# Kernel tuning notes

Measured on AMD Instinct MI355X. Metric: run time of the kernel, lower is better.

## Reference

```python
import jax, jax.numpy as jnp
import numpy as np

IN_F = 1024
OUT_F = 2048
BATCH = 1024
LAMBD = 0.2
TOL = 1e-4
MAX_ITERS = 100


def setup_inputs() -> dict:
    key = jax.random.key(0)
    kx, kw = jax.random.split(key)
    x = jax.random.normal(kx, (BATCH, IN_F), dtype=jnp.float32)
    # weight init exactly as in torch __init__: randn then column-wise (dim=0) L2 normalization
    w = jax.random.normal(kw, (OUT_F, IN_F), dtype=jnp.float32)
    w = w / jnp.linalg.norm(w, axis=0)  # norm over out_features, broadcast over columns
    A = w.T  # (in, out)
    M = A.T @ A + jnp.eye(OUT_F, dtype=jnp.float32)  # (out, out)
    M_inv = jnp.linalg.inv(M).T
    return {"x": x, "weight": w, "M_inv": M_inv}


def _softshrink(z, lambd):
    return jnp.sign(z) * jnp.maximum(jnp.abs(z) - lambd, 0.0)


def _basis_pursuit_admm(A_dot_b, M_inv, lambd=LAMBD, tol=TOL, max_iters=MAX_ITERS):
    # Mask-based equivalent of the torch dynamic-resizing loop: solved rows are
    # frozen instead of removed; v_solution captures v at the iteration a row converges.
    B, Mdim = A_dot_b.shape
    z = jnp.zeros((B, Mdim), dtype=A_dot_b.dtype)
    solved0 = jnp.zeros((B,), dtype=bool)
    init = (z, z, z, z, solved0)  # v, u, v_prev, v_solution, solved

    def step(carry, _):
        v, u, v_prev, v_sol, solved = carry
        b_eff = A_dot_b + v - u                      # (B, M)
        xk = b_eff @ M_inv                           # (B, M) @ (M, M)
        v_new = _softshrink(xk + u, lambd)
        u_new = u + xk - v_new
        # negligible_improvement on the updated v vs previous v
        dx = jnp.linalg.norm(v_new - v_prev, axis=1)
        xn = jnp.linalg.norm(v_new, axis=1)
        conv = (dx / xn) < tol
        newly = conv & (~solved)
        v_sol = jnp.where(newly[:, None], v_new, v_sol)
        frozen = solved[:, None]
        v = jnp.where(frozen, v, v_new)
        u = jnp.where(frozen, u, u_new)
        solved = solved | newly
        return (v, u, v, v_sol, solved), None

    (v, u, v_prev, v_sol, solved), _ = jax.lax.scan(step, init, None, length=max_iters)
    # Matches torch: rows still unsolved after max_iters keep their initial zero solution.
    return v_sol


def reference(x, weight, M_inv):
    input_shape = x.shape
    b = jax.lax.stop_gradient(x.reshape(x.shape[0], -1))  # x.detach() in torch
    A_dot_b = b @ weight.T                                 # b.matmul(A) with A = weight.T
    encoded = _basis_pursuit_admm(A_dot_b, M_inv)
    decoded = encoded @ weight
    return encoded, decoded.reshape(input_shape)
```

## Files before the change

kernel.cpp:

```cpp
#include <hip/hip_runtime.h>
#include <math.h>

#define BATCH 1024
#define IN_F  1024
#define OUT_F 2048
#define LAMBD 0.2f
#define TOL   1e-4f
#define MAX_ITERS 100

#define KSPLIT 4
#define KCHUNK (OUT_F / KSPLIT)
#define BSCALE 32.0f
#define BSCALE_INV 0.03125f

typedef _Float16 half8 __attribute__((ext_vector_type(8)));
typedef _Float16 half4 __attribute__((ext_vector_type(4)));
typedef float    floatx16 __attribute__((ext_vector_type(16)));
typedef unsigned char fp8_t;

#define GLOAD_LDS16(g, l) __builtin_amdgcn_global_load_lds(              \
    (const __attribute__((address_space(1))) void*)(g),                  \
    (__attribute__((address_space(3))) void*)(l), 16, 0, 0)

__device__ inline int pk4_fp8(float a, float b, float c, float d) {
    int w = __builtin_amdgcn_cvt_pk_fp8_f32(a, b, 0, false);
    w = __builtin_amdgcn_cvt_pk_fp8_f32(c, d, w, true);
    return w;
}
__device__ inline fp8_t enc_fp8(float a) {
    return (fp8_t)(__builtin_amdgcn_cvt_pk_fp8_f32(a, a, 0, false) & 0xff);
}
__device__ inline void cvt4_fp8(int w, float o[4]) {
    o[0] = __builtin_amdgcn_cvt_f32_fp8(w, 0);
    o[1] = __builtin_amdgcn_cvt_f32_fp8(w, 1);
    o[2] = __builtin_amdgcn_cvt_f32_fp8(w, 2);
    o[3] = __builtin_amdgcn_cvt_f32_fp8(w, 3);
}

__global__ void init_kernel(float4* __restrict__ v16, float4* __restrict__ u16,
                            float4* __restrict__ enc, int* __restrict__ solved) {
    const int i = blockIdx.x * blockDim.x + threadIdx.x;
    const float4 z = make_float4(0.f, 0.f, 0.f, 0.f);
    const int nh = BATCH * OUT_F / 8;
    const int n4 = BATCH * OUT_F / 4;
    if (i < nh) { v16[i] = z; u16[i] = z; }
    if (i < n4) enc[i] = z;
    if (i < BATCH) solved[i] = 0;
}

__global__ __launch_bounds__(256)
void cast_f16_kernel(const float* __restrict__ in, _Float16* __restrict__ out, int n) {
    const int i = (blockIdx.x * 256 + threadIdx.x) * 4;
    if (i < n) {
        const float4 f = *(const float4*)&in[i];
        half4 h;
        h[0] = (_Float16)f.x; h[1] = (_Float16)f.y;
        h[2] = (_Float16)f.z; h[3] = (_Float16)f.w;
        *(half4*)&out[i] = h;
    }
}

__global__ __launch_bounds__(256)
void transpose_w_kernel(const float* __restrict__ W, _Float16* __restrict__ WT) {
    __shared__ float tile[32][33];
    const int tid = threadIdx.x;
    const int row0 = blockIdx.y * 32;
    const int col0 = blockIdx.x * 32;
    const int r = tid >> 3;
    const int c4 = (tid & 7) * 4;
    const float4 b4 = *(const float4*)&W[(size_t)(row0 + r) * IN_F + col0 + c4];
    tile[r][c4 + 0] = b4.x; tile[r][c4 + 1] = b4.y;
    tile[r][c4 + 2] = b4.z; tile[r][c4 + 3] = b4.w;
    __syncthreads();
    half4 h;
#pragma unroll
    for (int j = 0; j < 4; ++j) h[j] = (_Float16)tile[c4 + j][r];
    *(half4*)&WT[(size_t)(col0 + r) * OUT_F + row0 + c4] = h;
}

__global__ __launch_bounds__(256)
void split_b_kernel(const float* __restrict__ B, fp8_t* __restrict__ BhT) {
    __shared__ float tile[32][33];
    const int tid = threadIdx.x;
    const int k0 = blockIdx.y * 32;
    const int n0 = blockIdx.x * 32;
    const int r = tid >> 3;
    const int c4 = (tid & 7) * 4;
    const float4 b4 = *(const float4*)&B[(size_t)(k0 + r) * OUT_F + n0 + c4];
    tile[r][c4 + 0] = b4.x; tile[r][c4 + 1] = b4.y;
    tile[r][c4 + 2] = b4.z; tile[r][c4 + 3] = b4.w;
    __syncthreads();
    const int w = pk4_fp8(tile[c4 + 0][r] * BSCALE, tile[c4 + 1][r] * BSCALE,
                          tile[c4 + 2][r] * BSCALE, tile[c4 + 3][r] * BSCALE);
    *(int*)&BhT[(size_t)(n0 + r) * OUT_F + k0 + c4] = w;
}

__global__ __launch_bounds__(256)
void mfma_nt_ab(const _Float16* __restrict__ A, const _Float16* __restrict__ B,
                fp8_t* __restrict__ Ab8, fp8_t* __restrict__ Ah,
                int N, int K) {
    __shared__ _Float16 sA[128 * 32];
    __shared__ _Float16 sB[128 * 32];
    const int tid = threadIdx.x;
    const int m0 = blockIdx.y * 128;
    const int n0 = blockIdx.x * 128;
    const int wv = tid >> 6, ln = tid & 63;
    const int half = ln >> 5, l31 = ln & 31;
    const int wm = (wv >> 1) * 64, wn = (wv & 1) * 64;
    const int r0 = tid >> 2, koff = (tid & 3) * 8;
    const size_t ga0 = (size_t)(m0 + r0) * K + koff;
    const size_t ga1 = (size_t)(m0 + r0 + 64) * K + koff;
    const size_t gb0 = (size_t)(n0 + r0) * K + koff;
    const size_t gb1 = (size_t)(n0 + r0 + 64) * K + koff;
    const int ldst0 = tid * 8, ldst1 = (256 + tid) * 8;

    floatx16 acc[2][2];
#pragma unroll
    for (int a = 0; a < 2; ++a)
#pragma unroll
        for (int b = 0; b < 2; ++b)
#pragma unroll
            for (int q = 0; q < 16; ++q) acc[a][b][q] = 0.f;

    for (int k = 0; k < K; k += 32) {
        __syncthreads();
        GLOAD_LDS16(A + ga0 + k, sA + ldst0);
        GLOAD_LDS16(A + ga1 + k, sA + ldst1);
        GLOAD_LDS16(B + gb0 + k, sB + ldst0);
        GLOAD_LDS16(B + gb1 + k, sB + ldst1);
        __syncthreads();
#pragma unroll
        for (int kk = 0; kk < 2; ++kk) {
            const int ko = kk * 16 + half * 8;
            const half8 a0 = *(const half8*)&sA[(wm + l31) * 32 + ko];
            const half8 a1 = *(const half8*)&sA[(wm + 32 + l31) * 32 + ko];
            const half8 b0 = *(const half8*)&sB[(wn + l31) * 32 + ko];
            const half8 b1 = *(const half8*)&sB[(wn + 32 + l31) * 32 + ko];
            acc[0][0] = __builtin_amdgcn_mfma_f32_32x32x16_f16(a0, b0, acc[0][0], 0, 0, 0);
            acc[0][1] = __builtin_amdgcn_mfma_f32_32x32x16_f16(a0, b1, acc[0][1], 0, 0, 0);
            acc[1][0] = __builtin_amdgcn_mfma_f32_32x32x16_f16(a1, b0, acc[1][0], 0, 0, 0);
            acc[1][1] = __builtin_amdgcn_mfma_f32_32x32x16_f16(a1, b1, acc[1][1], 0, 0, 0);
        }
    }
#pragma unroll
    for (int mm = 0; mm < 2; ++mm)
#pragma unroll
        for (int nn = 0; nn < 2; ++nn) {
            const int col = n0 + wn + nn * 32 + l31;
#pragma unroll
            for (int q = 0; q < 16; ++q) {
                const int row = m0 + wm + mm * 32 + (q & 3) + 8 * (q >> 2) + 4 * half;
                const size_t o = (size_t)row * N + col;
                const fp8_t e = enc_fp8(acc[mm][nn][q]);
                Ab8[o] = e;
                Ah[o] = e;
            }
        }
}

__global__ __launch_bounds__(256)
void mfma_nn_dec(const _Float16* __restrict__ A, const _Float16* __restrict__ B,
                 float* __restrict__ C, int N, int K) {
    __shared__ _Float16 sA[128 * 32];
    __shared__ _Float16 sB[128 * 32];
    const int tid = threadIdx.x;
    const int m0 = blockIdx.y * 128;
    const int n0 = blockIdx.x * 128;
    const int wv = tid >> 6, ln = tid & 63;
    const int half = ln >> 5, l31 = ln & 31;
    const int wm = (wv >> 1) * 64, wn = (wv & 1) * 64;
    const int r0 = tid >> 2, koff = (tid & 3) * 8;
    const size_t ga0 = (size_t)(m0 + r0) * K + koff;
    const size_t ga1 = (size_t)(m0 + r0 + 64) * K + koff;
    const size_t gb0 = (size_t)(n0 + r0) * K + koff;
    const size_t gb1 = (size_t)(n0 + r0 + 64) * K + koff;
    const int ldst0 = tid * 8, ldst1 = (256 + tid) * 8;

    floatx16 acc[2][2];
#pragma unroll
    for (int a = 0; a < 2; ++a)
#pragma unroll
        for (int b = 0; b < 2; ++b)
#pragma unroll
            for (int q = 0; q < 16; ++q) acc[a][b][q] = 0.f;

    for (int k = 0; k < K; k += 32) {
        __syncthreads();
        GLOAD_LDS16(A + ga0 + k, sA + ldst0);
        GLOAD_LDS16(A + ga1 + k, sA + ldst1);
        GLOAD_LDS16(B + gb0 + k, sB + ldst0);
        GLOAD_LDS16(B + gb1 + k, sB + ldst1);
        __syncthreads();
#pragma unroll
        for (int kk = 0; kk < 2; ++kk) {
            const int ko = kk * 16 + half * 8;
            const half8 a0 = *(const half8*)&sA[(wm + l31) * 32 + ko];
            const half8 a1 = *(const half8*)&sA[(wm + 32 + l31) * 32 + ko];
            const half8 b0 = *(const half8*)&sB[(wn + l31) * 32 + ko];
            const half8 b1 = *(const half8*)&sB[(wn + 32 + l31) * 32 + ko];
            acc[0][0] = __builtin_amdgcn_mfma_f32_32x32x16_f16(a0, b0, acc[0][0], 0, 0, 0);
            acc[0][1] = __builtin_amdgcn_mfma_f32_32x32x16_f16(a0, b1, acc[0][1], 0, 0, 0);
            acc[1][0] = __builtin_amdgcn_mfma_f32_32x32x16_f16(a1, b0, acc[1][0], 0, 0, 0);
            acc[1][1] = __builtin_amdgcn_mfma_f32_32x32x16_f16(a1, b1, acc[1][1], 0, 0, 0);
        }
    }
#pragma unroll
    for (int mm = 0; mm < 2; ++mm)
#pragma unroll
        for (int nn = 0; nn < 2; ++nn) {
            const int col = n0 + wn + nn * 32 + l31;
#pragma unroll
            for (int q = 0; q < 16; ++q) {
                const int row = m0 + wm + mm * 32 + (q & 3) + 8 * (q >> 2) + 4 * half;
                C[(size_t)row * N + col] = acc[mm][nn][q];
            }
        }
}

__global__ __launch_bounds__(256)
void xk_mfma(const fp8_t* __restrict__ Ah, const fp8_t* __restrict__ BhT,
             fp8_t* __restrict__ xkp, const int* __restrict__ solved) {
    __shared__ fp8_t smem[16384];
    fp8_t* sA = smem;
    fp8_t* sB = smem + 8192;
    const int tid = threadIdx.x;
    const int m0 = blockIdx.y * 128;
    const int n0 = blockIdx.x * 128;
    const int kz = blockIdx.z;
    constexpr size_t P = (size_t)BATCH * OUT_F;

    __shared__ int s_active;
    if (tid == 0) s_active = 0;
    __syncthreads();
    if (tid < 128 && solved[m0 + tid] == 0) s_active = 1;
    __syncthreads();
    if (!s_active) return;

    const int wv = tid >> 6;
    const int ln = tid & 63;
    const int half = ln >> 5;
    const int l31 = ln & 31;
    const int wm = (wv >> 1) * 64;
    const int wn = (wv & 1) * 64;

    const int r = tid & 127;
    const int c0 = tid >> 7;
    const fp8_t* gA = Ah  + (size_t)(m0 + r) * OUT_F + kz * KCHUNK;
    const fp8_t* gB = BhT + (size_t)(n0 + r) * OUT_F + kz * KCHUNK;
    fp8_t* lA0 = sA + (c0 * 128 + r) * 16;
    fp8_t* lA1 = sA + ((c0 + 2) * 128 + r) * 16;
    fp8_t* lB0 = sB + (c0 * 128 + r) * 16;
    fp8_t* lB1 = sB + ((c0 + 2) * 128 + r) * 16;

    floatx16 acc[2][2];
#pragma unroll
    for (int a = 0; a < 2; ++a)
#pragma unroll
        for (int b = 0; b < 2; ++b)
#pragma unroll
            for (int q = 0; q < 16; ++q) acc[a][b][q] = 0.f;

    const int ao0 = (wm + l31) * 16 + half * 8;
    const int ao1 = (wm + 32 + l31) * 16 + half * 8;
    const int bo0 = (wn + l31) * 16 + half * 8;
    const int bo1 = (wn + 32 + l31) * 16 + half * 8;

    for (int k = 0; k < KCHUNK; k += 64) {
        __syncthreads();
        GLOAD_LDS16(gA + k + c0 * 16, lA0);
        GLOAD_LDS16(gA + k + (c0 + 2) * 16, lA1);
        GLOAD_LDS16(gB + k + c0 * 16, lB0);
        GLOAD_LDS16(gB + k + (c0 + 2) * 16, lB1);
        __syncthreads();

#pragma unroll
        for (int kk = 0; kk < 4; ++kk) {
            const int cb = kk * 2048;
            const long long a0 = *(const long long*)&sA[cb + ao0];
            const long long a1 = *(const long long*)&sA[cb + ao1];
            const long long b0 = *(const long long*)&sB[cb + bo0];
            const long long b1 = *(const long long*)&sB[cb + bo1];
            acc[0][0] = __builtin_amdgcn_mfma_f32_32x32x16_fp8_fp8(a0, b0, acc[0][0], 0, 0, 0);
            acc[0][1] = __builtin_amdgcn_mfma_f32_32x32x16_fp8_fp8(a0, b1, acc[0][1], 0, 0, 0);
            acc[1][0] = __builtin_amdgcn_mfma_f32_32x32x16_fp8_fp8(a1, b0, acc[1][0], 0, 0, 0);
            acc[1][1] = __builtin_amdgcn_mfma_f32_32x32x16_fp8_fp8(a1, b1, acc[1][1], 0, 0, 0);
        }
    }

    __syncthreads();
#pragma unroll
    for (int mm = 0; mm < 2; ++mm)
#pragma unroll
        for (int nn = 0; nn < 2; ++nn) {
            const int lcol = wn + nn * 32 + l31;
#pragma unroll
            for (int q = 0; q < 16; ++q) {
                const int lrow = wm + mm * 32 + (q & 3) + 8 * (q >> 2) + 4 * half;
                smem[lrow * 128 + lcol] = enc_fp8(acc[mm][nn][q] * BSCALE_INV);
            }
        }
    __syncthreads();
    fp8_t* outp = xkp + kz * P + (size_t)m0 * OUT_F + n0;
#pragma unroll
    for (int s = 0; s < 4; ++s) {
        const int f = (s * 256 + tid) * 16;
        *(int4*)&outp[(size_t)(f >> 7) * OUT_F + (f & 127)] = *(const int4*)&smem[f];
    }
}

__global__ __launch_bounds__(256)
void update_kernel(const fp8_t* __restrict__ xkp, const fp8_t* __restrict__ Ab8,
                   _Float16* __restrict__ v, _Float16* __restrict__ u,
                   float* __restrict__ enc, fp8_t* __restrict__ Ah,
                   int* __restrict__ solved) {
    const int row = blockIdx.x;
    if (solved[row]) return;
    const int t = threadIdx.x;
    constexpr size_t P = (size_t)BATCH * OUT_F;

    const int c = t * 8;
    const size_t off = (size_t)row * OUT_F + c;
    const int2 q0 = *(const int2*)&xkp[off];
    const int2 q1 = *(const int2*)&xkp[P + off];
    const int2 q2 = *(const int2*)&xkp[2 * P + off];
    const int2 q3 = *(const int2*)&xkp[3 * P + off];
    const half8 u8 = *(const half8*)&u[off];
    const half8 v8 = *(const half8*)&v[off];
    const int2 ab2 = *(const int2*)&Ab8[off];

    float f0[4], f1[4], f2[4], f3[4], g0[4], g1[4], g2[4], g3[4];
    cvt4_fp8(q0.x, f0); cvt4_fp8(q1.x, f1); cvt4_fp8(q2.x, f2); cvt4_fp8(q3.x, f3);
    cvt4_fp8(q0.y, g0); cvt4_fp8(q1.y, g1); cvt4_fp8(q2.y, g2); cvt4_fp8(q3.y, g3);
    float ab0[4], ab1[4];
    cvt4_fp8(ab2.x, ab0); cvt4_fp8(ab2.y, ab1);
    float xs[8], abv[8];
#pragma unroll
    for (int j = 0; j < 4; ++j) {
        xs[j] = f0[j] + f1[j] + f2[j] + f3[j];
        xs[j + 4] = g0[j] + g1[j] + g2[j] + g3[j];
        abv[j] = ab0[j];
        abv[j + 4] = ab1[j];
    }

    float vn_all[8], ae[8];
    half8 vo, uo;
    float dx2 = 0.f, xn2 = 0.f;
#pragma unroll
    for (int j = 0; j < 8; ++j) {
        const float xk = xs[j];
        const float uv = (float)u8[j];
        const float vp = (float)v8[j];
        const float z = xk + uv;
        const float az = fabsf(z) - LAMBD;
        const float vnew = az > 0.f ? copysignf(az, z) : 0.f;
        const float unew = uv + xk - vnew;
        const float d = vnew - vp;
        dx2 += d * d;
        xn2 += vnew * vnew;
        vn_all[j] = vnew;
        vo[j] = (_Float16)vnew;
        uo[j] = (_Float16)unew;
        ae[j] = abv[j] + vnew - unew;
    }
    *(half8*)&v[off] = vo;
    *(half8*)&u[off] = uo;
    int2 ah;
    ah.x = pk4_fp8(ae[0], ae[1], ae[2], ae[3]);
    ah.y = pk4_fp8(ae[4], ae[5], ae[6], ae[7]);
    *(int2*)&Ah[off] = ah;

#pragma unroll
    for (int o = 32; o > 0; o >>= 1) {
        dx2 += __shfl_down(dx2, o);
        xn2 += __shfl_down(xn2, o);
    }
    __shared__ float sdx[4], sxn[4];
    __shared__ float s_conv;
    if ((t & 63) == 0) { sdx[t >> 6] = dx2; sxn[t >> 6] = xn2; }
    __syncthreads();
    if (t == 0) {
        const float dxt = sqrtf(sdx[0] + sdx[1] + sdx[2] + sdx[3]);
        const float xnt = sqrtf(sxn[0] + sxn[1] + sxn[2] + sxn[3]);
        const bool conv = (dxt / xnt) < TOL;
        s_conv = conv ? 1.f : 0.f;
        if (conv) solved[row] = 1;
    }
    __syncthreads();
    if (s_conv != 0.f) {
        *(float4*)&enc[off] = make_float4(vn_all[0], vn_all[1], vn_all[2], vn_all[3]);
        *(float4*)&enc[off + 4] = make_float4(vn_all[4], vn_all[5], vn_all[6], vn_all[7]);
    }
}

extern "C" void kernel_launch(void* const* d_in, const int* in_sizes, int n_in,
                              void* d_out, int out_size, void* d_ws, size_t ws_size,
                              hipStream_t stream) {
    (void)in_sizes; (void)n_in; (void)out_size; (void)ws_size;
    const float* x    = (const float*)d_in[0];
    const float* w    = (const float*)d_in[1];
    const float* Minv = (const float*)d_in[2];

    float* enc = (float*)d_out;
    float* dec = enc + (size_t)BATCH * OUT_F;

    constexpr size_t P = (size_t)BATCH * OUT_F;
    fp8_t* Ab8 = (fp8_t*)d_ws;
    _Float16* v   = (_Float16*)(Ab8 + P);
    _Float16* u   = v + P;
    _Float16* xh  = u + P;
    _Float16* wh  = xh + (size_t)BATCH * IN_F;
    _Float16* whT = wh + (size_t)OUT_F * IN_F;
    _Float16* ench = whT + (size_t)IN_F * OUT_F;
    fp8_t* Ah  = (fp8_t*)(ench + P);
    fp8_t* xkp = Ah + P;
    fp8_t* BhT = xkp + 4 * P;
    int* solved = (int*)(BhT + (size_t)OUT_F * OUT_F);

    {
        const int n = BATCH * OUT_F / 4;
        init_kernel<<<(n + 255) / 256, 256, 0, stream>>>(
            (float4*)v, (float4*)u, (float4*)enc, solved);
    }

    split_b_kernel<<<dim3(OUT_F / 32, OUT_F / 32), 256, 0, stream>>>(Minv, BhT);

    cast_f16_kernel<<<(BATCH * IN_F / 4 + 255) / 256, 256, 0, stream>>>(x, xh, BATCH * IN_F);
    cast_f16_kernel<<<(OUT_F * IN_F / 4 + 255) / 256, 256, 0, stream>>>(w, wh, OUT_F * IN_F);
    transpose_w_kernel<<<dim3(IN_F / 32, OUT_F / 32), 256, 0, stream>>>(w, whT);

    mfma_nt_ab<<<dim3(OUT_F / 128, BATCH / 128), 256, 0, stream>>>(
        xh, wh, Ab8, Ah, OUT_F, IN_F);

    for (int it = 0; it < MAX_ITERS; ++it) {
        xk_mfma<<<dim3(OUT_F / 128, BATCH / 128, KSPLIT), 256, 0, stream>>>(
            Ah, BhT, xkp, solved);
        update_kernel<<<BATCH, 256, 0, stream>>>(xkp, Ab8, v, u, enc, Ah, solved);
    }

    cast_f16_kernel<<<(BATCH * OUT_F / 4 + 255) / 256, 256, 0, stream>>>(enc, ench, BATCH * OUT_F);
    mfma_nn_dec<<<dim3(IN_F / 128, BATCH / 128), 256, 0, stream>>>(
        ench, whT, dec, IN_F, OUT_F);
}
```

Measured before the change: 2.261 ms.

## Compact unsolved rows into a list so the GEMM runs only on active tiles

The update kernel now builds a compacted, double-buffered list of unsolved batch rows and a count. Block 0 does this with a prefix-sum scan and pads the list to a multiple of 128. The xk GEMM gathers A rows through this list and launches only enough row-tiles to cover the active count. Before, a 128-row tile was skipped only if every row in it was solved. The cost is an indirect row gather, a serial compaction in one block, and a list that can lag by one iteration because block 0 reads `solved` while other blocks are still updating it. The per-row `solved` check in the update kernel keeps that lag from corrupting results.

```diff
diff --git a/kernel.cpp b/kernel.cpp
--- a/kernel.cpp
+++ b/kernel.cpp
@@ -38,14 +38,16 @@
 }
 
 __global__ void init_kernel(float4* __restrict__ v16, float4* __restrict__ u16,
-                            float4* __restrict__ enc, int* __restrict__ solved) {
+                            float4* __restrict__ enc, int* __restrict__ solved,
+                            int* __restrict__ list0, int* __restrict__ cnts) {
     const int i = blockIdx.x * blockDim.x + threadIdx.x;
     const float4 z = make_float4(0.f, 0.f, 0.f, 0.f);
     const int nh = BATCH * OUT_F / 8;
     const int n4 = BATCH * OUT_F / 4;
     if (i < nh) { v16[i] = z; u16[i] = z; }
     if (i < n4) enc[i] = z;
-    if (i < BATCH) solved[i] = 0;
+    if (i < BATCH) { solved[i] = 0; list0[i] = i; }
+    if (i < 2) cnts[i] = BATCH;
 }
 
 __global__ __launch_bounds__(256)
@@ -219,22 +221,19 @@
 
 __global__ __launch_bounds__(256)
 void xk_mfma(const fp8_t* __restrict__ Ah, const fp8_t* __restrict__ BhT,
-             fp8_t* __restrict__ xkp, const int* __restrict__ solved) {
+             fp8_t* __restrict__ xkp, const int* __restrict__ list_cur,
+             const int* __restrict__ cnt_cur) {
+    const int cnt = *cnt_cur;
+    const int m0 = blockIdx.y * 128;
+    if (m0 >= cnt) return;
+
     __shared__ fp8_t smem[16384];
     fp8_t* sA = smem;
     fp8_t* sB = smem + 8192;
     const int tid = threadIdx.x;
-    const int m0 = blockIdx.y * 128;
     const int n0 = blockIdx.x * 128;
     const int kz = blockIdx.z;
     constexpr size_t P = (size_t)BATCH * OUT_F;
-
-    __shared__ int s_active;
-    if (tid == 0) s_active = 0;
-    __syncthreads();
-    if (tid < 128 && solved[m0 + tid] == 0) s_active = 1;
-    __syncthreads();
-    if (!s_active) return;
 
     const int wv = tid >> 6;
     const int ln = tid & 63;
@@ -245,7 +244,8 @@
 
     const int r = tid & 127;
     const int c0 = tid >> 7;
-    const fp8_t* gA = Ah  + (size_t)(m0 + r) * OUT_F + kz * KCHUNK;
+    const int arow = list_cur[m0 + r];
+    const fp8_t* gA = Ah  + (size_t)arow * OUT_F + kz * KCHUNK;
     const fp8_t* gB = BhT + (size_t)(n0 + r) * OUT_F + kz * KCHUNK;
     fp8_t* lA0 = sA + (c0 * 128 + r) * 16;
     fp8_t* lA1 = sA + ((c0 + 2) * 128 + r) * 16;
@@ -312,83 +312,136 @@
 void update_kernel(const fp8_t* __restrict__ xkp, const fp8_t* __restrict__ Ab8,
                    _Float16* __restrict__ v, _Float16* __restrict__ u,
                    float* __restrict__ enc, fp8_t* __restrict__ Ah,
-                   int* __restrict__ solved) {
-    const int row = blockIdx.x;
-    if (solved[row]) return;
+                   int* __restrict__ solved,
+                   const int* __restrict__ list_cur, int* __restrict__ list_nxt,
+                   const int* __restrict__ cnt_cur, int* __restrict__ cnt_nxt) {
+    const int cnt = *cnt_cur;
+    const int p = blockIdx.x;
     const int t = threadIdx.x;
+    if (p >= cnt && p != 0) return;
     constexpr size_t P = (size_t)BATCH * OUT_F;
 
-    const int c = t * 8;
-    const size_t off = (size_t)row * OUT_F + c;
-    const int2 q0 = *(const int2*)&xkp[off];
-    const int2 q1 = *(const int2*)&xkp[P + off];
-    const int2 q2 = *(const int2*)&xkp[2 * P + off];
-    const int2 q3 = *(const int2*)&xkp[3 * P + off];
-    const half8 u8 = *(const half8*)&u[off];
-    const half8 v8 = *(const half8*)&v[off];
-    const int2 ab2 = *(const int2*)&Ab8[off];
-
-    float f0[4], f1[4], f2[4], f3[4], g0[4], g1[4], g2[4], g3[4];
-    cvt4_fp8(q0.x, f0); cvt4_fp8(q1.x, f1); cvt4_fp8(q2.x, f2); cvt4_fp8(q3.x, f3);
-    cvt4_fp8(q0.y, g0); cvt4_fp8(q1.y, g1); cvt4_fp8(q2.y, g2); cvt4_fp8(q3.y, g3);
-    float ab0[4], ab1[4];
-    cvt4_fp8(ab2.x, ab0); cvt4_fp8(ab2.y, ab1);
-    float xs[8], abv[8];
-#pragma unroll
-    for (int j = 0; j < 4; ++j) {
-        xs[j] = f0[j] + f1[j] + f2[j] + f3[j];
-        xs[j + 4] = g0[j] + g1[j] + g2[j] + g3[j];
-        abv[j] = ab0[j];
-        abv[j + 4] = ab1[j];
-    }
-
-    float vn_all[8], ae[8];
-    half8 vo, uo;
-    float dx2 = 0.f, xn2 = 0.f;
-#pragma unroll
-    for (int j = 0; j < 8; ++j) {
-        const float xk = xs[j];
-        const float uv = (float)u8[j];
-        const float vp = (float)v8[j];
-        const float z = xk + uv;
-        const float az = fabsf(z) - LAMBD;
-        const float vnew = az > 0.f ? copysignf(az, z) : 0.f;
-        const float unew = uv + xk - vnew;
-        const float d = vnew - vp;
-        dx2 += d * d;
-        xn2 += vnew * vnew;
-        vn_all[j] = vnew;
-        vo[j] = (_Float16)vnew;
-        uo[j] = (_Float16)unew;
-        ae[j] = abv[j] + vnew - unew;
-    }
-    *(half8*)&v[off] = vo;
-    *(half8*)&u[off] = uo;
-    int2 ah;
-    ah.x = pk4_fp8(ae[0], ae[1], ae[2], ae[3]);
-    ah.y = pk4_fp8(ae[4], ae[5], ae[6], ae[7]);
-    *(int2*)&Ah[off] = ah;
-
-#pragma unroll
-    for (int o = 32; o > 0; o >>= 1) {
-        dx2 += __shfl_down(dx2, o);
-        xn2 += __shfl_down(xn2, o);
-    }
     __shared__ float sdx[4], sxn[4];
     __shared__ float s_conv;
-    if ((t & 63) == 0) { sdx[t >> 6] = dx2; sxn[t >> 6] = xn2; }
-    __syncthreads();
-    if (t == 0) {
-        const float dxt = sqrtf(sdx[0] + sdx[1] + sdx[2] + sdx[3]);
-        const float xnt = sqrtf(sxn[0] + sxn[1] + sxn[2] + sxn[3]);
-        const bool conv = (dxt / xnt) < TOL;
-        s_conv = conv ? 1.f : 0.f;
-        if (conv) solved[row] = 1;
-    }
-    __syncthreads();
-    if (s_conv != 0.f) {
-        *(float4*)&enc[off] = make_float4(vn_all[0], vn_all[1], vn_all[2], vn_all[3]);
-        *(float4*)&enc[off + 4] = make_float4(vn_all[4], vn_all[5], vn_all[6], vn_all[7]);
+    __shared__ int wbase[5];
+
+    const bool dowork = (p < cnt);
+    int row = 0;
+    bool active = false;
+    if (dowork) {
+        row = list_cur[p];
+        active = (solved[row] == 0);
+    }
+
+    if (active) {
+        const int c = t * 8;
+        const size_t offp = (size_t)p * OUT_F + c;
+        const size_t off  = (size_t)row * OUT_F + c;
+        const int2 q0 = *(const int2*)&xkp[offp];
+        const int2 q1 = *(const int2*)&xkp[P + offp];
+        const int2 q2 = *(const int2*)&xkp[2 * P + offp];
+        const int2 q3 = *(const int2*)&xkp[3 * P + offp];
+        const half8 u8 = *(const half8*)&u[off];
+        const half8 v8 = *(const half8*)&v[off];
+        const int2 ab2 = *(const int2*)&Ab8[off];
+
+        float f0[4], f1[4], f2[4], f3[4], g0[4], g1[4], g2[4], g3[4];
+        cvt4_fp8(q0.x, f0); cvt4_fp8(q1.x, f1); cvt4_fp8(q2.x, f2); cvt4_fp8(q3.x, f3);
+        cvt4_fp8(q0.y, g0); cvt4_fp8(q1.y, g1); cvt4_fp8(q2.y, g2); cvt4_fp8(q3.y, g3);
+        float ab0[4], ab1[4];
+        cvt4_fp8(ab2.x, ab0); cvt4_fp8(ab2.y, ab1);
+        float xs[8], abv[8];
+#pragma unroll
+        for (int j = 0; j < 4; ++j) {
+            xs[j] = f0[j] + f1[j] + f2[j] + f3[j];
+            xs[j + 4] = g0[j] + g1[j] + g2[j] + g3[j];
+            abv[j] = ab0[j];
+            abv[j + 4] = ab1[j];
+        }
+
+        float vn_all[8], ae[8];
+        half8 vo, uo;
+        float dx2 = 0.f, xn2 = 0.f;
+#pragma unroll
+        for (int j = 0; j < 8; ++j) {
+            const float xk = xs[j];
+            const float uv = (float)u8[j];
+            const float vp = (float)v8[j];
+            const float z = xk + uv;
+            const float az = fabsf(z) - LAMBD;
+            const float vnew = az > 0.f ? copysignf(az, z) : 0.f;
+            const float unew = uv + xk - vnew;
+            const float d = vnew - vp;
+            dx2 += d * d;
+            xn2 += vnew * vnew;
+            vn_all[j] = vnew;
+            vo[j] = (_Float16)vnew;
+            uo[j] = (_Float16)unew;
+            ae[j] = abv[j] + vnew - unew;
+        }
+        *(half8*)&v[off] = vo;
+        *(half8*)&u[off] = uo;
+        int2 ah;
+        ah.x = pk4_fp8(ae[0], ae[1], ae[2], ae[3]);
+        ah.y = pk4_fp8(ae[4], ae[5], ae[6], ae[7]);
+        *(int2*)&Ah[off] = ah;
+
+#pragma unroll
+        for (int o = 32; o > 0; o >>= 1) {
+            dx2 += __shfl_down(dx2, o);
+            xn2 += __shfl_down(xn2, o);
+        }
+        if ((t & 63) == 0) { sdx[t >> 6] = dx2; sxn[t >> 6] = xn2; }
+        __syncthreads();
+        if (t == 0) {
+            const float dxt = sqrtf(sdx[0] + sdx[1] + sdx[2] + sdx[3]);
+            const float xnt = sqrtf(sxn[0] + sxn[1] + sxn[2] + sxn[3]);
+            const bool conv = (dxt / xnt) < TOL;
+            s_conv = conv ? 1.f : 0.f;
+            if (conv) solved[row] = 1;
+        }
+        __syncthreads();
+        if (s_conv != 0.f) {
+            *(float4*)&enc[off] = make_float4(vn_all[0], vn_all[1], vn_all[2], vn_all[3]);
+            *(float4*)&enc[off + 4] = make_float4(vn_all[4], vn_all[5], vn_all[6], vn_all[7]);
+        }
+    }
+
+    if (p == 0) {
+        const int lane = t & 63;
+        const int wv = t >> 6;
+        int m = 0;
+#pragma unroll
+        for (int j = 0; j < 4; ++j) {
+            const int rr = t * 4 + j;
+            if (solved[rr] == 0) m |= 1 << j;
+        }
+        const int c4 = __popc(m);
+        int inc = c4;
+#pragma unroll
+        for (int off = 1; off < 64; off <<= 1) {
+            const int x = __shfl_up(inc, off);
+            if (lane >= off) inc += x;
+        }
+        const int exc = inc - c4;
+        if (lane == 63) wbase[wv] = inc;
+        __syncthreads();
+        if (t == 0) {
+            int s = 0;
+#pragma unroll
+            for (int w = 0; w < 4; ++w) { const int x = wbase[w]; wbase[w] = s; s += x; }
+            wbase[4] = s;
+        }
+        __syncthreads();
+        int pos = wbase[wv] + exc;
+#pragma unroll
+        for (int j = 0; j < 4; ++j) {
+            if (m & (1 << j)) list_nxt[pos++] = t * 4 + j;
+        }
+        const int total = wbase[4];
+        if (t == 0) *cnt_nxt = total;
+        const int padc = (total + 127) & ~127;
+        for (int i = total + t; i < padc; i += 256) list_nxt[i] = 0;
     }
 }
 
@@ -416,10 +469,14 @@
     fp8_t* BhT = xkp + 4 * P;
     int* solved = (int*)(BhT + (size_t)OUT_F * OUT_F);
 
+    int* list0 = (int*)ench;
+    int* list1 = list0 + BATCH;
+    int* cnts  = list1 + BATCH;
+
     {
         const int n = BATCH * OUT_F / 4;
         init_kernel<<<(n + 255) / 256, 256, 0, stream>>>(
-            (float4*)v, (float4*)u, (float4*)enc, solved);
+            (float4*)v, (float4*)u, (float4*)enc, solved, list0, cnts);
     }
 
     split_b_kernel<<<dim3(OUT_F / 32, OUT_F / 32), 256, 0, stream>>>(Minv, BhT);
@@ -432,9 +489,15 @@
         xh, wh, Ab8, Ah, OUT_F, IN_F);
 
     for (int it = 0; it < MAX_ITERS; ++it) {
+        const int par = it & 1;
+        const int* lc = par ? list1 : list0;
+        int*       ln = par ? list0 : list1;
+        const int* cc = cnts + par;
+        int*       cn = cnts + (par ^ 1);
         xk_mfma<<<dim3(OUT_F / 128, BATCH / 128, KSPLIT), 256, 0, stream>>>(
-            Ah, BhT, xkp, solved);
-        update_kernel<<<BATCH, 256, 0, stream>>>(xkp, Ab8, v, u, enc, Ah, solved);
+            Ah, BhT, xkp, lc, cc);
+        update_kernel<<<BATCH, 256, 0, stream>>>(
+            xkp, Ab8, v, u, enc, Ah, solved, lc, ln, cc, cn);
     }
 
     cast_f16_kernel<<<(BATCH * OUT_F / 4 + 255) / 256, 256, 0, stream>>>(enc, ench, BATCH * OUT_F);
```

Result: slower. 2.330 ms (+3.0%).

## Double-buffer LDS in GEMM kernels and fuse setup kernels into one launch

Applied to the files above, without the earlier changes.

Adds double-buffered shared-memory tiles to the three MFMA GEMM kernels, so the next K-slice is prefetched with global_load_lds while the current one is computed, and one barrier per step replaces two. It also merges the init, cast, transpose and Minv-to-fp8 preprocessing kernels into a single launch that branches on block index. The goal is to hide global load latency in the 100-iteration xk GEMM loop and cut launch overhead. In exchange it doubles LDS use per block, which may lower occupancy.

```diff
diff --git a/kernel.cpp b/kernel.cpp
--- a/kernel.cpp
+++ b/kernel.cpp
@@ -37,15 +37,84 @@
     o[3] = __builtin_amdgcn_cvt_f32_fp8(w, 3);
 }
 
-__global__ void init_kernel(float4* __restrict__ v16, float4* __restrict__ u16,
-                            float4* __restrict__ enc, int* __restrict__ solved) {
-    const int i = blockIdx.x * blockDim.x + threadIdx.x;
-    const float4 z = make_float4(0.f, 0.f, 0.f, 0.f);
-    const int nh = BATCH * OUT_F / 8;
-    const int n4 = BATCH * OUT_F / 4;
-    if (i < nh) { v16[i] = z; u16[i] = z; }
-    if (i < n4) enc[i] = z;
-    if (i < BATCH) solved[i] = 0;
+#define NB_INIT 2048
+#define NB_CX   1024
+#define NB_CW   2048
+#define NB_TW   2048
+#define NB_SB   4096
+#define NB_TOTAL (NB_INIT + NB_CX + NB_CW + NB_TW + NB_SB)
+
+__global__ __launch_bounds__(256)
+void setup_kernel(const float* __restrict__ x, const float* __restrict__ w,
+                  const float* __restrict__ Minv,
+                  float4* __restrict__ v16, float4* __restrict__ u16,
+                  float4* __restrict__ enc4, int* __restrict__ solved,
+                  _Float16* __restrict__ xh, _Float16* __restrict__ wh,
+                  _Float16* __restrict__ whT, fp8_t* __restrict__ BhT) {
+    const int b = blockIdx.x;
+    const int tid = threadIdx.x;
+    __shared__ float tile[32][33];
+
+    if (b < NB_INIT) {
+        const int idx = b * 256 + tid;
+        const float4 z = make_float4(0.f, 0.f, 0.f, 0.f);
+        enc4[idx] = z;
+        if (idx < BATCH * OUT_F / 8) { v16[idx] = z; u16[idx] = z; }
+        if (idx < BATCH) solved[idx] = 0;
+        return;
+    }
+    if (b < NB_INIT + NB_CX) {
+        const int i = ((b - NB_INIT) * 256 + tid) * 4;
+        const float4 f = *(const float4*)&x[i];
+        half4 h;
+        h[0] = (_Float16)f.x; h[1] = (_Float16)f.y;
+        h[2] = (_Float16)f.z; h[3] = (_Float16)f.w;
+        *(half4*)&xh[i] = h;
+        return;
+    }
+    if (b < NB_INIT + NB_CX + NB_CW) {
+        const int i = ((b - NB_INIT - NB_CX) * 256 + tid) * 4;
+        const float4 f = *(const float4*)&w[i];
+        half4 h;
+        h[0] = (_Float16)f.x; h[1] = (_Float16)f.y;
+        h[2] = (_Float16)f.z; h[3] = (_Float16)f.w;
+        *(half4*)&wh[i] = h;
+        return;
+    }
+    if (b < NB_INIT + NB_CX + NB_CW + NB_TW) {
+        const int lb = b - NB_INIT - NB_CX - NB_CW;
+        const int bx = lb & 31;
+        const int by = lb >> 5;
+        const int row0 = by * 32;
+        const int col0 = bx * 32;
+        const int r = tid >> 3;
+        const int c4 = (tid & 7) * 4;
+        const float4 b4 = *(const float4*)&w[(size_t)(row0 + r) * IN_F + col0 + c4];
+        tile[r][c4 + 0] = b4.x; tile[r][c4 + 1] = b4.y;
+        tile[r][c4 + 2] = b4.z; tile[r][c4 + 3] = b4.w;
+        __syncthreads();
+        half4 h;
+#pragma unroll
+        for (int j = 0; j < 4; ++j) h[j] = (_Float16)tile[c4 + j][r];
+        *(half4*)&whT[(size_t)(col0 + r) * OUT_F + row0 + c4] = h;
+        return;
+    }
+    {
+        const int lb = b - NB_INIT - NB_CX - NB_CW - NB_TW;
+        const int bx = lb & 63;
+        const int by = lb >> 6;
+        const int k0 = by * 32;
+        const int n0 = bx * 32;
+        const int r = tid >> 3;
+        const int c4 = (tid & 7) * 4;
+        const float4 b4 = *(const float4*)&Minv[(size_t)(k0 + r) * OUT_F + n0 + c4];
+        tile[r][c4 + 0] = b4.x; tile[r][c4 + 1] = b4.y;
+        tile[r][c4 + 2] = b4.z; tile[r][c4 + 3] = b4.w;
+        __syncthreads();
+        const int wrd = pk4_fp8(tile[c4 + 0][r] * BSCALE, tile[c4 + 1][r] * BSCALE,
+                                tile[c4 + 2][r] * BSCALE, tile[c4 + 3][r] * BSCALE);
+        *(int*)&BhT[(size_t)(n0 + r) * OUT_F + k0 + c4] = wrd;
+    }
 }
 
 __global__ __launch_bounds__(256)
@@ -61,46 +130,10 @@
 }
 
 __global__ __launch_bounds__(256)
-void transpose_w_kernel(const float* __restrict__ W, _Float16* __restrict__ WT) {
-    __shared__ float tile[32][33];
-    const int tid = threadIdx.x;
-    const int row0 = blockIdx.y * 32;
-    const int col0 = blockIdx.x * 32;
-    const int r = tid >> 3;
-    const int c4 = (tid & 7) * 4;
-    const float4 b4 = *(const float4*)&W[(size_t)(row0 + r) * IN_F + col0 + c4];
-    tile[r][c4 + 0] = b4.x; tile[r][c4 + 1] = b4.y;
-    tile[r][c4 + 2] = b4.z; tile[r][c4 + 3] = b4.w;
-    __syncthreads();
-    half4 h;
-#pragma unroll
-    for (int j = 0; j < 4; ++j) h[j] = (_Float16)tile[c4 + j][r];
-    *(half4*)&WT[(size_t)(col0 + r) * OUT_F + row0 + c4] = h;
-}
-
-__global__ __launch_bounds__(256)
-void split_b_kernel(const float* __restrict__ B, fp8_t* __restrict__ BhT) {
-    __shared__ float tile[32][33];
-    const int tid = threadIdx.x;
-    const int k0 = blockIdx.y * 32;
-    const int n0 = blockIdx.x * 32;
-    const int r = tid >> 3;
-    const int c4 = (tid & 7) * 4;
-    const float4 b4 = *(const float4*)&B[(size_t)(k0 + r) * OUT_F + n0 + c4];
-    tile[r][c4 + 0] = b4.x; tile[r][c4 + 1] = b4.y;
-    tile[r][c4 + 2] = b4.z; tile[r][c4 + 3] = b4.w;
-    __syncthreads();
-    const int w = pk4_fp8(tile[c4 + 0][r] * BSCALE, tile[c4 + 1][r] * BSCALE,
-                          tile[c4 + 2][r] * BSCALE, tile[c4 + 3][r] * BSCALE);
-    *(int*)&BhT[(size_t)(n0 + r) * OUT_F + k0 + c4] = w;
-}
-
-__global__ __launch_bounds__(256)
 void mfma_nt_ab(const _Float16* __restrict__ A, const _Float16* __restrict__ B,
                 fp8_t* __restrict__ Ab8, fp8_t* __restrict__ Ah,
                 int N, int K) {
-    __shared__ _Float16 sA[128 * 32];
-    __shared__ _Float16 sB[128 * 32];
+    __shared__ _Float16 sAB[2][8192];
     const int tid = threadIdx.x;
     const int m0 = blockIdx.y * 128;
     const int n0 = blockIdx.x * 128;
@@ -122,13 +155,30 @@
 #pragma unroll
             for (int q = 0; q < 16; ++q) acc[a][b][q] = 0.f;
 
-    for (int k = 0; k < K; k += 32) {
-        __syncthreads();
-        GLOAD_LDS16(A + ga0 + k, sA + ldst0);
-        GLOAD_LDS16(A + ga1 + k, sA + ldst1);
-        GLOAD_LDS16(B + gb0 + k, sB + ldst0);
-        GLOAD_LDS16(B + gb1 + k, sB + ldst1);
-        __syncthreads();
+    {
+        _Float16* bufA = sAB[0];
+        _Float16* bufB = sAB[0] + 4096;
+        GLOAD_LDS16(A + ga0, bufA + ldst0);
+        GLOAD_LDS16(A + ga1, bufA + ldst1);
+        GLOAD_LDS16(B + gb0, bufB + ldst0);
+        GLOAD_LDS16(B + gb1, bufB + ldst1);
+    }
+    __syncthreads();
+
+    const int nsteps = K >> 5;
+    for (int s = 0; s < nsteps; ++s) {
+        const int cur = s & 1;
+        if (s + 1 < nsteps) {
+            const int k = (s + 1) * 32;
+            _Float16* bufA = sAB[cur ^ 1];
+            _Float16* bufB = sAB[cur ^ 1] + 4096;
+            GLOAD_LDS16(A + ga0 + k, bufA + ldst0);
+            GLOAD_LDS16(A + ga1 + k, bufA + ldst1);
+            GLOAD_LDS16(B + gb0 + k, bufB + ldst0);
+            GLOAD_LDS16(B + gb1 + k, bufB + ldst1);
+        }
+        const _Float16* sA = sAB[cur];
+        const _Float16* sB = sAB[cur] + 4096;
 #pragma unroll
         for (int kk = 0; kk < 2; ++kk) {
             const int ko = kk * 16 + half * 8;
@@ -141,6 +191,7 @@
             acc[1][0] = __builtin_amdgcn_mfma_f32_32x32x16_f16(a1, b0, acc[1][0], 0, 0, 0);
             acc[1][1] = __builtin_amdgcn_mfma_f32_32x32x16_f16(a1, b1, acc[1][1], 0, 0, 0);
         }
+        __syncthreads();
     }
 #pragma unroll
     for (int mm = 0; mm < 2; ++mm)
@@ -161,8 +212,7 @@
 __global__ __launch_bounds__(256)
 void mfma_nn_dec(const _Float16* __restrict__ A, const _Float16* __restrict__ B,
                  float* __restrict__ C, int N, int K) {
-    __shared__ _Float16 sA[128 * 32];
-    __shared__ _Float16 sB[128 * 32];
+    __shared__ _Float16 sAB[2][8192];
     const int tid = threadIdx.x;
     const int m0 = blockIdx.y * 128;
     const int n0 = blockIdx.x * 128;
@@ -184,13 +234,30 @@
 #pragma unroll
             for (int q = 0; q < 16; ++q) acc[a][b][q] = 0.f;
 
-    for (int k = 0; k < K; k += 32) {
-        __syncthreads();
-        GLOAD_LDS16(A + ga0 + k, sA + ldst0);
-        GLOAD_LDS16(A + ga1 + k, sA + ldst1);
-        GLOAD_LDS16(B + gb0 + k, sB + ldst0);
-        GLOAD_LDS16(B + gb1 + k, sB + ldst1);
-        __syncthreads();
+    {
+        _Float16* bufA = sAB[0];
+        _Float16* bufB = sAB[0] + 4096;
+        GLOAD_LDS16(A + ga0, bufA + ldst0);
+        GLOAD_LDS16(A + ga1, bufA + ldst1);
+        GLOAD_LDS16(B + gb0, bufB + ldst0);
+        GLOAD_LDS16(B + gb1, bufB + ldst1);
+    }
+    __syncthreads();
+
+    const int nsteps = K >> 5;
+    for (int s = 0; s < nsteps; ++s) {
+        const int cur = s & 1;
+        if (s + 1 < nsteps) {
+            const int k = (s + 1) * 32;
+            _Float16* bufA = sAB[cur ^ 1];
+            _Float16* bufB = sAB[cur ^ 1] + 4096;
+            GLOAD_LDS16(A + ga0 + k, bufA + ldst0);
+            GLOAD_LDS16(A + ga1 + k, bufA + ldst1);
+            GLOAD_LDS16(B + gb0 + k, bufB + ldst0);
+            GLOAD_LDS16(B + gb1 + k, bufB + ldst1);
+        }
+        const _Float16* sA = sAB[cur];
+        const _Float16* sB = sAB[cur] + 4096;
 #pragma unroll
         for (int kk = 0; kk < 2; ++kk) {
             const int ko = kk * 16 + half * 8;
@@ -203,6 +270,7 @@
             acc[1][0] = __builtin_amdgcn_mfma_f32_32x32x16_f16(a1, b0, acc[1][0], 0, 0, 0);
             acc[1][1] = __builtin_amdgcn_mfma_f32_32x32x16_f16(a1, b1, acc[1][1], 0, 0, 0);
         }
+        __syncthreads();
     }
 #pragma unroll
     for (int mm = 0; mm < 2; ++mm)
@@ -220,9 +288,7 @@
 __global__ __launch_bounds__(256)
 void xk_mfma(const fp8_t* __restrict__ Ah, const fp8_t* __restrict__ BhT,
              fp8_t* __restrict__ xkp, const int* __restrict__ solved) {
-    __shared__ fp8_t smem[16384];
-    fp8_t* sA = smem;
-    fp8_t* sB = smem + 8192;
+    __shared__ fp8_t smem[2][16384];
     const int tid = threadIdx.x;
     const int m0 = blockIdx.y * 128;
     const int n0 = blockIdx.x * 128;
@@ -247,10 +313,8 @@
     const int c0 = tid >> 7;
     const fp8_t* gA = Ah  + (size_t)(m0 + r) * OUT_F + kz * KCHUNK;
     const fp8_t* gB = BhT + (size_t)(n0 + r) * OUT_F + kz * KCHUNK;
-    fp8_t* lA0 = sA + (c0 * 128 + r) * 16;
-    fp8_t* lA1 = sA + ((c0 + 2) * 128 + r) * 16;
-    fp8_t* lB0 = sB + (c0 * 128 + r) * 16;
-    fp8_t* lB1 = sB + ((c0 + 2) * 128 + r) * 16;
+    const int dA0 = (c0 * 128 + r) * 16;
+    const int dA1 = ((c0 + 2) * 128 + r) * 16;
 
     floatx16 acc[2][2];
 #pragma unroll
@@ -265,14 +329,30 @@
     const int bo0 = (wn + l31) * 16 + half * 8;
     const int bo1 = (wn + 32 + l31) * 16 + half * 8;
 
-    for (int k = 0; k < KCHUNK; k += 64) {
-        __syncthreads();
-        GLOAD_LDS16(gA + k + c0 * 16, lA0);
-        GLOAD_LDS16(gA + k + (c0 + 2) * 16, lA1);
-        GLOAD_LDS16(gB + k + c0 * 16, lB0);
-        GLOAD_LDS16(gB + k + (c0 + 2) * 16, lB1);
-        __syncthreads();
-
+    {
+        fp8_t* sA = smem[0];
+        fp8_t* sB = smem[0] + 8192;
+        GLOAD_LDS16(gA + c0 * 16, sA + dA0);
+        GLOAD_LDS16(gA + (c0 + 2) * 16, sA + dA1);
+        GLOAD_LDS16(gB + c0 * 16, sB + dA0);
+        GLOAD_LDS16(gB + (c0 + 2) * 16, sB + dA1);
+    }
+    __syncthreads();
+
+#pragma unroll 1
+    for (int s = 0; s < KCHUNK / 64; ++s) {
+        const int cur = s & 1;
+        if (s + 1 < KCHUNK / 64) {
+            const int k = (s + 1) * 64;
+            fp8_t* nA = smem[cur ^ 1];
+            fp8_t* nB = smem[cur ^ 1] + 8192;
+            GLOAD_LDS16(gA + k + c0 * 16, nA + dA0);
+            GLOAD_LDS16(gA + k + (c0 + 2) * 16, nA + dA1);
+            GLOAD_LDS16(gB + k + c0 * 16, nB + dA0);
+            GLOAD_LDS16(gB + k + (c0 + 2) * 16, nB + dA1);
+        }
+        const fp8_t* sA = smem[cur];
+        const fp8_t* sB = smem[cur] + 8192;
 #pragma unroll
         for (int kk = 0; kk < 4; ++kk) {
             const int cb = kk * 2048;
@@ -285,9 +365,10 @@
             acc[1][0] = __builtin_amdgcn_mfma_f32_32x32x16_fp8_fp8(a1, b0, acc[1][0], 0, 0, 0);
             acc[1][1] = __builtin_amdgcn_mfma_f32_32x32x16_fp8_fp8(a1, b1, acc[1][1], 0, 0, 0);
         }
-    }
-
-    __syncthreads();
+        __syncthreads();
+    }
+
+    fp8_t* sm = smem[0];
 #pragma unroll
     for (int mm = 0; mm < 2; ++mm)
 #pragma unroll
@@ -296,15 +377,15 @@
 #pragma unroll
             for (int q = 0; q < 16; ++q) {
                 const int lrow = wm + mm * 32 + (q & 3) + 8 * (q >> 2) + 4 * half;
-                smem[lrow * 128 + lcol] = enc_fp8(acc[mm][nn][q] * BSCALE_INV);
+                sm[lrow * 128 + lcol] = enc_fp8(acc[mm][nn][q] * BSCALE_INV);
             }
         }
     __syncthreads();
     fp8_t* outp = xkp + kz * P + (size_t)m0 * OUT_F + n0;
 #pragma unroll
-    for (int s = 0; s < 4; ++s) {
-        const int f = (s * 256 + tid) * 16;
-        *(int4*)&outp[(size_t)(f >> 7) * OUT_F + (f & 127)] = *(const int4*)&smem[f];
+    for (int s4 = 0; s4 < 4; ++s4) {
+        const int f = (s4 * 256 + tid) * 16;
+        *(int4*)&outp[(size_t)(f >> 7) * OUT_F + (f & 127)] = *(const int4*)&sm[f];
     }
 }
 
@@ -416,17 +497,9 @@
     fp8_t* BhT = xkp + 4 * P;
     int* solved = (int*)(BhT + (size_t)OUT_F * OUT_F);
 
-    {
-        const int n = BATCH * OUT_F / 4;
-        init_kernel<<<(n + 255) / 256, 256, 0, stream>>>(
-            (float4*)v, (float4*)u, (float4*)enc, solved);
-    }
-
-    split_b_kernel<<<dim3(OUT_F / 32, OUT_F / 32), 256, 0, stream>>>(Minv, BhT);
-
-    cast_f16_kernel<<<(BATCH * IN_F / 4 + 255) / 256, 256, 0, stream>>>(x, xh, BATCH * IN_F);
-    cast_f16_kernel<<<(OUT_F * IN_F / 4 + 255) / 256, 256, 0, stream>>>(w, wh, OUT_F * IN_F);
-    transpose_w_kernel<<<dim3(IN_F / 32, OUT_F / 32), 256, 0, stream>>>(w, whT);
+    setup_kernel<<<NB_TOTAL, 256, 0, stream>>>(
+        x, w, Minv, (float4*)v, (float4*)u, (float4*)enc, solved,
+        xh, wh, whT, BhT);
 
     mfma_nt_ab<<<dim3(OUT_F / 128, BATCH / 128), 256, 0, stream>>>(
         xh, wh, Ab8, Ah, OUT_F, IN_F);
```

New measurement: 2.313 ms. 1.02x slower.

## Fuse setup kernels and replace per-block solved scan with stripe activity flags

Applied to the files above, without the earlier changes.

Merges the init, cast, transpose and Minv split kernels into a single setup kernel with block-range dispatch, cutting launch count. In the iteration loop, xk_mfma no longer scans 128 solved flags with two barriers per block. Instead it reads a per-128-row stripe activity flag that update_kernel sets when a row is still unsolved, using double-buffered flag arrays. This trades a small flag-write protocol, and stripe_act aliasing the ench buffer, for less per-block overhead. Since 100 iterations dominate and GEMM work is unchanged, the expected effect is small.

```diff
diff --git a/kernel.cpp b/kernel.cpp
--- a/kernel.cpp
+++ b/kernel.cpp
@@ -37,15 +37,86 @@
     o[3] = __builtin_amdgcn_cvt_f32_fp8(w, 3);
 }
 
-__global__ void init_kernel(float4* __restrict__ v16, float4* __restrict__ u16,
-                            float4* __restrict__ enc, int* __restrict__ solved) {
-    const int i = blockIdx.x * blockDim.x + threadIdx.x;
-    const float4 z = make_float4(0.f, 0.f, 0.f, 0.f);
-    const int nh = BATCH * OUT_F / 8;
-    const int n4 = BATCH * OUT_F / 4;
-    if (i < nh) { v16[i] = z; u16[i] = z; }
-    if (i < n4) enc[i] = z;
-    if (i < BATCH) solved[i] = 0;
+#define NB_INIT 2048
+#define NB_CX   1024
+#define NB_CW   2048
+#define NB_TW   2048
+#define NB_SB   4096
+#define NB_TOTAL (NB_INIT + NB_CX + NB_CW + NB_TW + NB_SB)
+
+__global__ __launch_bounds__(256)
+void setup_kernel(const float* __restrict__ x, const float* __restrict__ w,
+                  const float* __restrict__ Minv,
+                  float4* __restrict__ v16, float4* __restrict__ u16,
+                  float4* __restrict__ enc4, int* __restrict__ solved,
+                  int* __restrict__ stripe_act,
+                  _Float16* __restrict__ xh, _Float16* __restrict__ wh,
+                  _Float16* __restrict__ whT, fp8_t* __restrict__ BhT) {
+    const int b = blockIdx.x;
+    const int tid = threadIdx.x;
+    __shared__ float tile[32][33];
+
+    if (b < NB_INIT) {
+        const int idx = b * 256 + tid;
+        const float4 z = make_float4(0.f, 0.f, 0.f, 0.f);
+        enc4[idx] = z;
+        if (idx < BATCH * OUT_F / 8) { v16[idx] = z; u16[idx] = z; }
+        if (idx < BATCH) solved[idx] = 0;
+        if (idx < 16) stripe_act[idx] = (idx < 8) ? 1 : 0;
+        return;
+    }
+    if (b < NB_INIT + NB_CX) {
+        const int i = ((b - NB_INIT) * 256 + tid) * 4;
+        const float4 f = *(const float4*)&x[i];
+        half4 h;
+        h[0] = (_Float16)f.x; h[1] = (_Float16)f.y;
+        h[2] = (_Float16)f.z; h[3] = (_Float16)f.w;
+        *(half4*)&xh[i] = h;
+        return;
+    }
+    if (b < NB_INIT + NB_CX + NB_CW) {
+        const int i = ((b - NB_INIT - NB_CX) * 256 + tid) * 4;
+        const float4 f = *(const float4*)&w[i];
+        half4 h;
+        h[0] = (_Float16)f.x; h[1] = (_Float16)f.y;
+        h[2] = (_Float16)f.z; h[3] = (_Float16)f.w;
+        *(half4*)&wh[i] = h;
+        return;
+    }
+    if (b < NB_INIT + NB_CX + NB_CW + NB_TW) {
+        const int lb = b - NB_INIT - NB_CX - NB_CW;
+        const int bx = lb & 31;
+        const int by = lb >> 5;
+        const int row0 = by * 32;
+        const int col0 = bx * 32;
+        const int r = tid >> 3;
+        const int c4 = (tid & 7) * 4;
+        const float4 b4 = *(const float4*)&w[(size_t)(row0 + r) * IN_F + col0 + c4];
+        tile[r][c4 + 0] = b4.x; tile[r][c4 + 1] = b4.y;
+        tile[r][c4 + 2] = b4.z; tile[r][c4 + 3] = b4.w;
+        __syncthreads();
+        half4 h;
+#pragma unroll
+        for (int j = 0; j < 4; ++j) h[j] = (_Float16)tile[c4 + j][r];
+        *(half4*)&whT[(size_t)(col0 + r) * OUT_F + row0 + c4] = h;
+        return;
+    }
+    {
+        const int lb = b - NB_INIT - NB_CX - NB_CW - NB_TW;
+        const int bx = lb & 63;
+        const int by = lb >> 6;
+        const int k0 = by * 32;
+        const int n0 = bx * 32;
+        const int r = tid >> 3;
+        const int c4 = (tid & 7) * 4;
+        const float4 b4 = *(const float4*)&Minv[(size_t)(k0 + r) * OUT_F + n0 + c4];
+        tile[r][c4 + 0] = b4.x; tile[r][c4 + 1] = b4.y;
+        tile[r][c4 + 2] = b4.z; tile[r][c4 + 3] = b4.w;
+        __syncthreads();
+        const int wrd = pk4_fp8(tile[c4 + 0][r] * BSCALE, tile[c4 + 1][r] * BSCALE,
+                                tile[c4 + 2][r] * BSCALE, tile[c4 + 3][r] * BSCALE);
+        *(int*)&BhT[(size_t)(n0 + r) * OUT_F + k0 + c4] = wrd;
+    }
 }
 
 __global__ __launch_bounds__(256)
@@ -58,41 +129,6 @@
         h[2] = (_Float16)f.z; h[3] = (_Float16)f.w;
         *(half4*)&out[i] = h;
     }
-}
-
-__global__ __launch_bounds__(256)
-void transpose_w_kernel(const float* __restrict__ W, _Float16* __restrict__ WT) {
-    __shared__ float tile[32][33];
-    const int tid = threadIdx.x;
-    const int row0 = blockIdx.y * 32;
-    const int col0 = blockIdx.x * 32;
-    const int r = tid >> 3;
-    const int c4 = (tid & 7) * 4;
-    const float4 b4 = *(const float4*)&W[(size_t)(row0 + r) * IN_F + col0 + c4];
-    tile[r][c4 + 0] = b4.x; tile[r][c4 + 1] = b4.y;
-    tile[r][c4 + 2] = b4.z; tile[r][c4 + 3] = b4.w;
-    __syncthreads();
-    half4 h;
-#pragma unroll
-    for (int j = 0; j < 4; ++j) h[j] = (_Float16)tile[c4 + j][r];
-    *(half4*)&WT[(size_t)(col0 + r) * OUT_F + row0 + c4] = h;
-}
-
-__global__ __launch_bounds__(256)
-void split_b_kernel(const float* __restrict__ B, fp8_t* __restrict__ BhT) {
-    __shared__ float tile[32][33];
-    const int tid = threadIdx.x;
-    const int k0 = blockIdx.y * 32;
-    const int n0 = blockIdx.x * 32;
-    const int r = tid >> 3;
-    const int c4 = (tid & 7) * 4;
-    const float4 b4 = *(const float4*)&B[(size_t)(k0 + r) * OUT_F + n0 + c4];
-    tile[r][c4 + 0] = b4.x; tile[r][c4 + 1] = b4.y;
-    tile[r][c4 + 2] = b4.z; tile[r][c4 + 3] = b4.w;
-    __syncthreads();
-    const int w = pk4_fp8(tile[c4 + 0][r] * BSCALE, tile[c4 + 1][r] * BSCALE,
-                          tile[c4 + 2][r] * BSCALE, tile[c4 + 3][r] * BSCALE);
-    *(int*)&BhT[(size_t)(n0 + r) * OUT_F + k0 + c4] = w;
 }
 
 __global__ __launch_bounds__(256)
@@ -219,22 +255,19 @@
 
 __global__ __launch_bounds__(256)
 void xk_mfma(const fp8_t* __restrict__ Ah, const fp8_t* __restrict__ BhT,
-             fp8_t* __restrict__ xkp, const int* __restrict__ solved) {
+             fp8_t* __restrict__ xkp, const int* __restrict__ stripe_cur,
+             int* __restrict__ stripe_nxt) {
+    const int tid = threadIdx.x;
+    if (blockIdx.x == 0 && blockIdx.z == 0 && tid < 8) stripe_nxt[tid] = 0;
+    if (stripe_cur[blockIdx.y] == 0) return;
+
     __shared__ fp8_t smem[16384];
     fp8_t* sA = smem;
     fp8_t* sB = smem + 8192;
-    const int tid = threadIdx.x;
     const int m0 = blockIdx.y * 128;
     const int n0 = blockIdx.x * 128;
     const int kz = blockIdx.z;
     constexpr size_t P = (size_t)BATCH * OUT_F;
-
-    __shared__ int s_active;
-    if (tid == 0) s_active = 0;
-    __syncthreads();
-    if (tid < 128 && solved[m0 + tid] == 0) s_active = 1;
-    __syncthreads();
-    if (!s_active) return;
 
     const int wv = tid >> 6;
     const int ln = tid & 63;
@@ -312,7 +345,7 @@
 void update_kernel(const fp8_t* __restrict__ xkp, const fp8_t* __restrict__ Ab8,
                    _Float16* __restrict__ v, _Float16* __restrict__ u,
                    float* __restrict__ enc, fp8_t* __restrict__ Ah,
-                   int* __restrict__ solved) {
+                   int* __restrict__ solved, int* __restrict__ stripe_nxt) {
     const int row = blockIdx.x;
     if (solved[row]) return;
     const int t = threadIdx.x;
@@ -384,6 +417,7 @@
         const bool conv = (dxt / xnt) < TOL;
         s_conv = conv ? 1.f : 0.f;
         if (conv) solved[row] = 1;
+        else      stripe_nxt[row >> 7] = 1;
     }
     __syncthreads();
     if (s_conv != 0.f) {
@@ -416,25 +450,21 @@
     fp8_t* BhT = xkp + 4 * P;
     int* solved = (int*)(BhT + (size_t)OUT_F * OUT_F);
 
-    {
-        const int n = BATCH * OUT_F / 4;
-        init_kernel<<<(n + 255) / 256, 256, 0, stream>>>(
-            (float4*)v, (float4*)u, (float4*)enc, solved);
-    }
-
-    split_b_kernel<<<dim3(OUT_F / 32, OUT_F / 32), 256, 0, stream>>>(Minv, BhT);
-
-    cast_f16_kernel<<<(BATCH * IN_F / 4 + 255) / 256, 256, 0, stream>>>(x, xh, BATCH * IN_F);
-    cast_f16_kernel<<<(OUT_F * IN_F / 4 + 255) / 256, 256, 0, stream>>>(w, wh, OUT_F * IN_F);
-    transpose_w_kernel<<<dim3(IN_F / 32, OUT_F / 32), 256, 0, stream>>>(w, whT);
+    int* stripe_act = (int*)ench;
+
+    setup_kernel<<<NB_TOTAL, 256, 0, stream>>>(
+        x, w, Minv, (float4*)v, (float4*)u, (float4*)enc, solved, stripe_act,
+        xh, wh, whT, BhT);
 
     mfma_nt_ab<<<dim3(OUT_F / 128, BATCH / 128), 256, 0, stream>>>(
         xh, wh, Ab8, Ah, OUT_F, IN_F);
 
     for (int it = 0; it < MAX_ITERS; ++it) {
+        const int par = it & 1;
         xk_mfma<<<dim3(OUT_F / 128, BATCH / 128, KSPLIT), 256, 0, stream>>>(
-            Ah, BhT, xkp, solved);
-        update_kernel<<<BATCH, 256, 0, stream>>>(xkp, Ab8, v, u, enc, Ah, solved);
+            Ah, BhT, xkp, stripe_act + par * 8, stripe_act + (par ^ 1) * 8);
+        update_kernel<<<BATCH, 256, 0, stream>>>(
+            xkp, Ab8, v, u, enc, Ah, solved, stripe_act + (par ^ 1) * 8);
     }
 
     cast_f16_kernel<<<(BATCH * OUT_F / 4 + 255) / 256, 256, 0, stream>>>(enc, ench, BATCH * OUT_F);
```

Measured after the change: 2.271 ms. About the same (+0.4%).
